# Kernel optimization log

Hardware: AMD Instinct MI355X
Metric: run time of the kernel (lower is better)

Reference implementation:

```python
import jax, jax.numpy as jnp
import numpy as np

B, S, E, H = 4, 2048, 1024, 16
D = E // H  # head_dim = 64


def setup_inputs() -> dict:
    key = jax.random.key(0)
    k1, k2, k3 = jax.random.split(key, 3)
    x = jax.random.normal(k1, (B, S, E), dtype=jnp.float32)
    w_attn = jax.random.normal(k2, (E, 3 * E), dtype=jnp.float32) * (E ** -0.5)
    b_attn = jnp.zeros((3 * E,), dtype=jnp.float32)
    w_out = jax.random.normal(k3, (E, E), dtype=jnp.float32) * (E ** -0.5)
    b_out = jnp.zeros((E,), dtype=jnp.float32)
    return {"x": x, "w_attn": w_attn, "b_attn": b_attn, "w_out": w_out, "b_out": b_out}


def reference(x, w_attn, b_attn, w_out, b_out):
    b, s, e = x.shape
    qkv = x @ w_attn + b_attn                      # [b, s, 3e]
    q, k, v = jnp.split(qkv, 3, axis=2)
    q = q.reshape(b, s, H, D)
    k = k.reshape(b, s, H, D)
    v = v.reshape(b, s, H, D)
    energy = jnp.einsum('nqhd,nkhd->nhqk', q, k)   # [b, H, s, s]
    causal = jnp.tril(jnp.ones((s, s), dtype=bool))
    energy = jnp.where(causal, energy, -jnp.inf)
    scale = jnp.sqrt(jnp.float32(D))
    attn = jax.nn.softmax(energy / scale, axis=-1)  # dropout_rate=0.0 -> identity
    out = jnp.einsum('nhql,nlhd->nqhd', attn, v).reshape(b, s, e)
    return out @ w_out + b_out
```

## Files before the change

### kernel.cpp

```cpp
#include <hip/hip_runtime.h>

typedef short bf16x8 __attribute__((ext_vector_type(8)));
typedef float f32x4 __attribute__((ext_vector_type(4)));
typedef float f32x16 __attribute__((ext_vector_type(16)));
typedef float float4v __attribute__((ext_vector_type(4)));
typedef short short4v __attribute__((ext_vector_type(4)));
typedef unsigned uint2v __attribute__((ext_vector_type(2)));
typedef unsigned uint4v __attribute__((ext_vector_type(4)));

#define B_ 4
#define S_ 2048
#define E_ 1024
#define H_ 16
#define D_ 64
#define M_ (B_*S_)
#define N1_ (3*E_)

__device__ inline short f2bs(float f) {
    unsigned u = __builtin_bit_cast(unsigned, f);
    unsigned r = u + 0x7fffu + ((u >> 16) & 1u);
    return (short)(r >> 16);
}
__device__ inline float exp2a(float x) {
    float r; asm("v_exp_f32 %0, %1" : "=v"(r) : "v"(x)); return r;
}
__device__ inline unsigned cvtpk(float a, float b) {
    unsigned r; asm("v_cvt_pk_bf16_f32 %0, %1, %2" : "=v"(r) : "v"(a), "v"(b)); return r;
}

__device__ inline const __attribute__((address_space(1))) void* gas(const void* p) {
    return (const __attribute__((address_space(1))) void*)p;
}
__device__ inline __attribute__((address_space(3))) void* las(void* p) {
    return (__attribute__((address_space(3))) void*)p;
}

__global__ void convert_f32_bf16(const float* __restrict__ in, short* __restrict__ out, int n) {
    int tid = blockIdx.x * blockDim.x + threadIdx.x;
    int stride = gridDim.x * blockDim.x;
    for (int i = tid * 4; i < n; i += stride * 4) {
        float4v v = *(const float4v*)&in[i];
        short4v o;
        o[0] = f2bs(v[0]); o[1] = f2bs(v[1]); o[2] = f2bs(v[2]); o[3] = f2bs(v[3]);
        *(short4v*)&out[i] = o;
    }
}

__global__ void transpose_convert(const float* __restrict__ in, short* __restrict__ out,
                                  int rows, int cols) {
    __shared__ float t[32][33];
    int bx = blockIdx.x * 32;
    int by = blockIdx.y * 32;
    int tx = threadIdx.x, ty = threadIdx.y;
#pragma unroll
    for (int i = 0; i < 4; ++i)
        t[ty + i * 8][tx] = in[(size_t)(by + ty + i * 8) * cols + bx + tx];
    __syncthreads();
#pragma unroll
    for (int i = 0; i < 4; ++i)
        out[(size_t)(bx + ty + i * 8) * rows + by + tx] = f2bs(t[tx][ty + i * 8]);
}

#define MFMA16(Q) \
    _Pragma("unroll") for (int mf = 0; mf < 2; ++mf) \
    _Pragma("unroll") for (int nf = 0; nf < 4; ++nf) { \
        acc[(Q)*2+mf][nf] = __builtin_amdgcn_mfma_f32_16x16x32_bf16(af[mf][0], bfrag[nf][0], acc[(Q)*2+mf][nf], 0, 0, 0); \
        acc[(Q)*2+mf][nf] = __builtin_amdgcn_mfma_f32_16x16x32_bf16(af[mf][1], bfrag[nf][1], acc[(Q)*2+mf][nf], 0, 0, 0); \
    }

#define PHASE(Q, STAGE_STMT, WAITV) do { \
    bf16x8 af[2][2]; \
    _Pragma("unroll") for (int mf = 0; mf < 2; ++mf) \
    _Pragma("unroll") for (int ks = 0; ks < 2; ++ks) { \
        int r = (Q)*32 + mf*16 + li; \
        af[mf][ks] = *(const bf16x8*)(lA + r*128 + ((ks*64 + g*16) ^ ((r & 7) << 4))); \
    } \
    STAGE_STMT; \
    __builtin_amdgcn_s_barrier(); \
    asm volatile("s_waitcnt lgkmcnt(0)" ::: "memory"); \
    __builtin_amdgcn_sched_barrier(0); \
    __builtin_amdgcn_s_setprio(1); \
    MFMA16(Q); \
    __builtin_amdgcn_s_setprio(0); \
    WAITV; \
    __builtin_amdgcn_s_barrier(); \
} while (0)

#define VMW(n) asm volatile("s_waitcnt vmcnt(" #n ")" ::: "memory")
#define NOP_ ((void)0)

__global__ __launch_bounds__(512, 2) void gemm256_qkv(
    const short* __restrict__ A, const short* __restrict__ Bt,
    const float* __restrict__ bias,
    short* __restrict__ Qb, short* __restrict__ Kb, short* __restrict__ Vt) {
    __shared__ __attribute__((aligned(16))) short lds[2][2][2][8192];
    const int tid = threadIdx.x;
    const int lane = tid & 63;
    const int wid = tid >> 6;
    const int li = lane & 15, g = lane >> 4;
    const int wr = wid >> 2, wc = wid & 3;
    const int Kdim = E_;
    const int NT = Kdim >> 6;

    const int id = blockIdx.x;
    const int swz = (id & 7) * 48 + (id >> 3);
    const int bx = swz % 12, by = swz / 12;
    const int row0 = by * 256, col0 = bx * 256;

    const int rstage = wid * 8 + (lane >> 3);
    const int cstage = (((lane & 7) ^ ((lane >> 3) & 7)) << 4);

    auto stageA = [&](int buf, int kt, int seg) {
#pragma unroll
        for (int h = 0; h < 2; ++h) {
            const char* src = (const char*)A +
                ((size_t)(row0 + h * 128 + seg * 64 + rstage) * Kdim + kt * 64) * 2 + cstage;
            char* dst = (char*)&lds[buf][0][h][0] + seg * 8192 + wid * 1024;
            __builtin_amdgcn_global_load_lds(gas(src), las(dst), 16, 0, 0);
        }
    };
    auto stageB = [&](int buf, int kt, int h) {
#pragma unroll
        for (int seg = 0; seg < 2; ++seg) {
            const char* src = (const char*)Bt +
                ((size_t)(col0 + h * 128 + seg * 64 + rstage) * Kdim + kt * 64) * 2 + cstage;
            char* dst = (char*)&lds[buf][1][h][0] + seg * 8192 + wid * 1024;
            __builtin_amdgcn_global_load_lds(gas(src), las(dst), 16, 0, 0);
        }
    };

    f32x4 acc[8][4];
#pragma unroll
    for (int m = 0; m < 8; ++m)
#pragma unroll
        for (int n = 0; n < 4; ++n) acc[m][n] = (f32x4){0.f, 0.f, 0.f, 0.f};

    stageB(0, 0, 0);
    stageB(0, 0, 1);
    stageA(0, 0, 0);
    stageA(0, 0, 1);
    asm volatile("s_waitcnt vmcnt(0)" ::: "memory");
    __syncthreads();

    const int bc = (wc & 1) * 64;
    for (int t = 0; t < NT; ++t) {
        const int cur = t & 1;
        const int nb = cur ^ 1;
        const int tn = t + 1;
        const bool st = (tn < NT);
        const char* lA = (const char*)&lds[cur][0][wr][0];
        const char* lB = (const char*)&lds[cur][1][wc >> 1][0];

        bf16x8 bfrag[4][2];
#pragma unroll
        for (int nf = 0; nf < 4; ++nf)
#pragma unroll
            for (int ks = 0; ks < 2; ++ks) {
                int r = bc + nf * 16 + li;
                bfrag[nf][ks] = *(const bf16x8*)(lB + r * 128 + ((ks * 64 + g * 16) ^ ((r & 7) << 4)));
            }
        if (st) {
            PHASE(0, stageB(nb, tn, 0), NOP_);
            PHASE(1, stageB(nb, tn, 1), VMW(4));
            PHASE(2, stageA(nb, tn, 0), NOP_);
            PHASE(3, stageA(nb, tn, 1), VMW(2));
        } else {
            PHASE(0, NOP_, NOP_);
            PHASE(1, NOP_, VMW(0));
            PHASE(2, NOP_, NOP_);
            PHASE(3, NOP_, NOP_);
        }
    }

    if (col0 < 2048) {
        short* Dst = (col0 < 1024) ? Qb : Kb;
#pragma unroll
        for (int nf = 0; nf < 4; ++nf) {
            int ncolg = col0 + wc * 64 + nf * 16 + li;
            float bv = bias[ncolg];
            int ncol = ncolg & 1023;
#pragma unroll
            for (int mi = 0; mi < 8; ++mi) {
                int rbase = row0 + wr * 128 + mi * 16 + 4 * g;
#pragma unroll
                for (int j = 0; j < 4; ++j)
                    Dst[(size_t)(rbase + j) * E_ + ncol] = f2bs(acc[mi][nf][j] + bv);
            }
        }
    } else {
#pragma unroll
        for (int nf = 0; nf < 4; ++nf) {
            int ncolg = col0 + wc * 64 + nf * 16 + li;
            float bv = bias[ncolg];
            int rem = ncolg & 1023;
            int h = rem >> 6, d = rem & 63;
#pragma unroll
            for (int mi = 0; mi < 8; ++mi) {
                int s0 = row0 + wr * 128 + mi * 16 + 4 * g;
                int bb2 = s0 >> 11;
                int ss = s0 & 2047;
                uint2v p;
                p[0] = cvtpk(acc[mi][nf][0] + bv, acc[mi][nf][1] + bv);
                p[1] = cvtpk(acc[mi][nf][2] + bv, acc[mi][nf][3] + bv);
                *(uint2v*)&Vt[((size_t)(bb2 * H_ + h) * D_ + d) * S_ + ss] = p;
            }
        }
    }
}

__global__ __launch_bounds__(256, 2) void gemm_bt_out(
    const short* __restrict__ A, const short* __restrict__ Bt,
    const float* __restrict__ bias, float* __restrict__ Cf,
    int Kdim, int Ndim) {
    __shared__ __attribute__((aligned(16))) short As[128 * 32];
    __shared__ __attribute__((aligned(16))) short Bs[128 * 32];
    const int lane = threadIdx.x & 63;
    const int wv = threadIdx.x >> 6;
    const int row0 = blockIdx.y * 128;
    const int col0 = blockIdx.x * 128;
    const int wr = (wv >> 1) * 64;
    const int wc = (wv & 1) * 64;
    const int li = lane & 15;
    const int g = lane >> 4;
    const int lr = lane >> 2;
    const int lk = (lane & 3) * 8;

    f32x4 acc[4][4];
#pragma unroll
    for (int m = 0; m < 4; ++m)
#pragma unroll
        for (int n = 0; n < 4; ++n) acc[m][n] = (f32x4){0.f, 0.f, 0.f, 0.f};

    for (int k0 = 0; k0 < Kdim; k0 += 32) {
#pragma unroll
        for (int i = 0; i < 2; ++i) {
            int cc = wv * 2 + i;
            const short* ga = A + (size_t)(row0 + cc * 16 + lr) * Kdim + k0 + lk;
            __builtin_amdgcn_global_load_lds(gas(ga), las(&As[cc * 512]), 16, 0, 0);
            const short* gb = Bt + (size_t)(col0 + cc * 16 + lr) * Kdim + k0 + lk;
            __builtin_amdgcn_global_load_lds(gas(gb), las(&Bs[cc * 512]), 16, 0, 0);
        }
        __syncthreads();
        bf16x8 af[4], bfr[4];
#pragma unroll
        for (int m = 0; m < 4; ++m) af[m] = *(const bf16x8*)&As[(wr + 16 * m + li) * 32 + g * 8];
#pragma unroll
        for (int n = 0; n < 4; ++n) bfr[n] = *(const bf16x8*)&Bs[(wc + 16 * n + li) * 32 + g * 8];
#pragma unroll
        for (int m = 0; m < 4; ++m)
#pragma unroll
            for (int n = 0; n < 4; ++n)
                acc[m][n] = __builtin_amdgcn_mfma_f32_16x16x32_bf16(af[m], bfr[n], acc[m][n], 0, 0, 0);
        __syncthreads();
    }

#pragma unroll
    for (int n = 0; n < 4; ++n) {
        int ncol = col0 + wc + 16 * n + li;
        float bv = bias[ncol];
#pragma unroll
        for (int m = 0; m < 4; ++m) {
            int rbase = row0 + wr + 16 * m + 4 * g;
#pragma unroll
            for (int j = 0; j < 4; ++j)
                Cf[(size_t)(rbase + j) * Ndim + ncol] = acc[m][n][j] + bv;
        }
    }
}

__global__ __launch_bounds__(256, 4) void attn_kernel(
    const short* __restrict__ Qb, const short* __restrict__ Kb,
    const short* __restrict__ Vt, short* __restrict__ Ob) {
    __shared__ __attribute__((aligned(16))) short Kl[4096];
    __shared__ __attribute__((aligned(16))) short Vl[4096];
    const int lane = threadIdx.x & 63;
    const int wv = threadIdx.x >> 6;
    const int l31 = lane & 31;
    const int hi = lane >> 5;
    const int id = blockIdx.x;
    const int xcd = id & 7;
    const int r_ = id >> 3;
    const int qt = 15 - (r_ >> 3);
    const int bh = xcd * 8 + (r_ & 7);
    const int bb = bh >> 4, hh = bh & 15;
    const short* Qh = Qb + (size_t)bb * (S_ * E_) + hh * 64;
    const short* Kh = Kb + (size_t)bb * (S_ * E_) + hh * 64;
    const short* Vh = Vt + (size_t)bh * (D_ * S_);
    const float CEXP = 0.18033688011112042f;

    const int rstage = wv * 8 + (lane >> 3);
    const int cstage = (((lane & 7) ^ ((lane >> 3) & 7)) << 4);

    const int q0w = qt * 128 + wv * 32;
    const int q = q0w + l31;

    bf16x8 qf[4];
#pragma unroll
    for (int c = 0; c < 4; ++c)
        qf[c] = *(const bf16x8*)&Qh[(size_t)q * E_ + c * 16 + hi * 8];

    f32x16 acc[2];
#pragma unroll
    for (int d = 0; d < 2; ++d)
#pragma unroll
        for (int r = 0; r < 16; ++r) acc[d][r] = 0.f;
    float m = -3e38f, mC = 0.f, l = 0.f;

    const int nw = (q0w + 95) >> 6;
    const int nt = (qt * 128 + 191) >> 6;

    for (int it = 0; it < nt; ++it) {
        const int kt0 = it * 64;
#pragma unroll
        for (int half = 0; half < 2; ++half) {
            const char* gk = (const char*)(Kh + (size_t)(kt0 + half * 32 + rstage) * E_) + cstage;
            __builtin_amdgcn_global_load_lds(gas(gk), las((char*)Kl + half * 4096 + wv * 1024), 16, 0, 0);
            const char* gv = (const char*)Vh + (size_t)(half * 32 + rstage) * (S_ * 2) + (size_t)kt0 * 2 + cstage;
            __builtin_amdgcn_global_load_lds(gas(gv), las((char*)Vl + half * 4096 + wv * 1024), 16, 0, 0);
        }
        __syncthreads();
        if (it < nw) {
#pragma unroll
            for (int s = 0; s < 2; ++s) {
                const int ktl = kt0 + s * 32;
                if (ktl > q0w + 31) continue;
                f32x16 sc;
#pragma unroll
                for (int r = 0; r < 16; ++r) sc[r] = 0.f;
#pragma unroll
                for (int c = 0; c < 4; ++c) {
                    const int row = s * 32 + l31;
                    bf16x8 kf = *(const bf16x8*)((const char*)Kl + row * 128 +
                                                 ((c * 32 + hi * 16) ^ ((row & 7) << 4)));
                    sc = __builtin_amdgcn_mfma_f32_32x32x16_bf16(kf, qf[c], sc, 0, 0, 0);
                }
                if (ktl + 31 > q0w) {
                    const int kb = ktl + 4 * hi;
#pragma unroll
                    for (int r = 0; r < 16; ++r) {
                        int key = kb + (r & 3) + 8 * (r >> 2);
                        sc[r] = (key > q) ? -3e38f : sc[r];
                    }
                }
                float t0 = fmaxf(sc[0], sc[1]), t1 = fmaxf(sc[2], sc[3]);
                float t2 = fmaxf(sc[4], sc[5]), t3 = fmaxf(sc[6], sc[7]);
                float t4 = fmaxf(sc[8], sc[9]), t5 = fmaxf(sc[10], sc[11]);
                float t6 = fmaxf(sc[12], sc[13]), t7 = fmaxf(sc[14], sc[15]);
                float tm = fmaxf(fmaxf(fmaxf(t0, t1), fmaxf(t2, t3)),
                                 fmaxf(fmaxf(t4, t5), fmaxf(t6, t7)));
                tm = fmaxf(tm, __shfl_xor(tm, 32, 64));
                bool need = (tm > m);
                if (__ballot((int)need) != 0ull) {
                    float mn = fmaxf(m, tm);
                    float sf = exp2a((m - mn) * CEXP);
                    m = mn; mC = mn * CEXP;
                    l *= sf;
#pragma unroll
                    for (int d = 0; d < 2; ++d)
#pragma unroll
                        for (int r = 0; r < 16; ++r) acc[d][r] *= sf;
                }
                float p[16];
#pragma unroll
                for (int r = 0; r < 16; ++r) p[r] = exp2a(fmaf(sc[r], CEXP, -mC));
                float s0 = (p[0] + p[1]) + (p[2] + p[3]);
                float s1 = (p[4] + p[5]) + (p[6] + p[7]);
                float s2 = (p[8] + p[9]) + (p[10] + p[11]);
                float s3 = (p[12] + p[13]) + (p[14] + p[15]);
                float ls = (s0 + s1) + (s2 + s3);
                ls += __shfl_xor(ls, 32, 64);
                l += ls;
                unsigned W0 = cvtpk(p[0], p[1]),  W1 = cvtpk(p[2], p[3]);
                unsigned W2 = cvtpk(p[4], p[5]),  W3 = cvtpk(p[6], p[7]);
                unsigned W4 = cvtpk(p[8], p[9]),  W5 = cvtpk(p[10], p[11]);
                unsigned W6 = cvtpk(p[12], p[13]), W7 = cvtpk(p[14], p[15]);
                unsigned xW0 = __shfl_xor(W0, 32, 64), xW1 = __shfl_xor(W1, 32, 64);
                unsigned xW2 = __shfl_xor(W2, 32, 64), xW3 = __shfl_xor(W3, 32, 64);
                unsigned xW4 = __shfl_xor(W4, 32, 64), xW5 = __shfl_xor(W5, 32, 64);
                unsigned xW6 = __shfl_xor(W6, 32, 64), xW7 = __shfl_xor(W7, 32, 64);
                const bool lo = (hi == 0);
                uint4v u1, u2;
                u1[0] = lo ? W0 : xW2;  u1[1] = lo ? W1 : xW3;
                u1[2] = lo ? xW0 : W2;  u1[3] = lo ? xW1 : W3;
                u2[0] = lo ? W4 : xW6;  u2[1] = lo ? W5 : xW7;
                u2[2] = lo ? xW4 : W6;  u2[3] = lo ? xW5 : W7;
                bf16x8 pf1 = __builtin_bit_cast(bf16x8, u1);
                bf16x8 pf2 = __builtin_bit_cast(bf16x8, u2);
#pragma unroll
                for (int db = 0; db < 2; ++db) {
                    const int row = db * 32 + l31;
                    const int rsw = (row & 7) << 4;
                    bf16x8 vf0 = *(const bf16x8*)((const char*)Vl + row * 128 +
                                                  ((s * 64 + hi * 16) ^ rsw));
                    bf16x8 vf1 = *(const bf16x8*)((const char*)Vl + row * 128 +
                                                  ((s * 64 + 32 + hi * 16) ^ rsw));
                    acc[db] = __builtin_amdgcn_mfma_f32_32x32x16_bf16(vf0, pf1, acc[db], 0, 0, 0);
                    acc[db] = __builtin_amdgcn_mfma_f32_32x32x16_bf16(vf1, pf2, acc[db], 0, 0, 0);
                }
            }
        }
        __syncthreads();
    }

    float rl = __builtin_amdgcn_rcpf(l);
    short* orow = Ob + ((size_t)(bb * S_ + q)) * E_ + hh * 64;
#pragma unroll
    for (int db = 0; db < 2; ++db)
#pragma unroll
        for (int rb = 0; rb < 4; ++rb) {
            uint2v pk;
            pk[0] = cvtpk(acc[db][rb * 4 + 0] * rl, acc[db][rb * 4 + 1] * rl);
            pk[1] = cvtpk(acc[db][rb * 4 + 2] * rl, acc[db][rb * 4 + 3] * rl);
            *(uint2v*)&orow[db * 32 + rb * 8 + hi * 4] = pk;
        }
}

extern "C" void kernel_launch(void* const* d_in, const int* in_sizes, int n_in,
                              void* d_out, int out_size, void* d_ws, size_t ws_size,
                              hipStream_t stream) {
    const float* x      = (const float*)d_in[0];
    const float* w_attn = (const float*)d_in[1];
    const float* b_attn = (const float*)d_in[2];
    const float* w_out  = (const float*)d_in[3];
    const float* b_out  = (const float*)d_in[4];
    float* out = (float*)d_out;

    char* ws = (char*)d_ws;
    short* Xbf  = (short*)(ws);
    short* Wat  = (short*)(ws + (16ull << 20));
    short* Wot  = (short*)(ws + (22ull << 20));
    short* Qb   = (short*)(ws + (24ull << 20));
    short* Kb   = (short*)(ws + (40ull << 20));
    short* Vt   = (short*)(ws + (56ull << 20));
    short* Obuf = Xbf;

    convert_f32_bf16<<<2048, 256, 0, stream>>>(x, Xbf, M_ * E_);
    transpose_convert<<<dim3(N1_ / 32, E_ / 32), dim3(32, 8), 0, stream>>>(w_attn, Wat, E_, N1_);
    transpose_convert<<<dim3(E_ / 32, E_ / 32), dim3(32, 8), 0, stream>>>(w_out, Wot, E_, E_);

    gemm256_qkv<<<384, 512, 0, stream>>>(Xbf, Wat, b_attn, Qb, Kb, Vt);

    attn_kernel<<<1024, 256, 0, stream>>>(Qb, Kb, Vt, Obuf);

    gemm_bt_out<<<dim3(E_ / 128, M_ / 128), 256, 0, stream>>>(
        Obuf, Wot, b_out, out, E_, E_);
}
```

Before: 184.3 us.

## Process 64-key tile in one softmax step with lazy max rescaling

The attention inner loop now computes scores for both 32-key halves of the 64-key tile together. It does one max reduction and one online-softmax update per tile instead of one per half, then issues all PV MFMAs back to back. The rescale condition is relaxed to trigger only when the new max exceeds the running max by more than 16, which skips most accumulator rescales. The trade-offs are that fully masked second halves are no longer skipped, register pressure rises, and unrescaled exponents can grow to about 2^(16*CEXP) before a rescale.

```diff
diff --git a/kernel.cpp b/kernel.cpp
--- a/kernel.cpp
+++ b/kernel.cpp
@@ -320,83 +320,95 @@
         }
         __syncthreads();
         if (it < nw) {
+            f32x16 sc0, sc1;
+#pragma unroll
+            for (int r = 0; r < 16; ++r) { sc0[r] = 0.f; sc1[r] = 0.f; }
+#pragma unroll
+            for (int c = 0; c < 4; ++c) {
+                const int r0 = l31, r1 = 32 + l31;
+                bf16x8 kf0 = *(const bf16x8*)((const char*)Kl + r0 * 128 +
+                                              ((c * 32 + hi * 16) ^ ((r0 & 7) << 4)));
+                bf16x8 kf1 = *(const bf16x8*)((const char*)Kl + r1 * 128 +
+                                              ((c * 32 + hi * 16) ^ ((r1 & 7) << 4)));
+                sc0 = __builtin_amdgcn_mfma_f32_32x32x16_bf16(kf0, qf[c], sc0, 0, 0, 0);
+                sc1 = __builtin_amdgcn_mfma_f32_32x32x16_bf16(kf1, qf[c], sc1, 0, 0, 0);
+            }
+            if (kt0 + 63 > q0w) {
+                const int kb = kt0 + 4 * hi;
+#pragma unroll
+                for (int r = 0; r < 16; ++r) {
+                    int key = kb + (r & 3) + 8 * (r >> 2);
+                    sc0[r] = (key > q) ? -3e38f : sc0[r];
+                    sc1[r] = (key + 32 > q) ? -3e38f : sc1[r];
+                }
+            }
+            float tmx[8];
+#pragma unroll
+            for (int r = 0; r < 8; ++r)
+                tmx[r] = fmaxf(fmaxf(sc0[2 * r], sc0[2 * r + 1]),
+                               fmaxf(sc1[2 * r], sc1[2 * r + 1]));
+            float tm = fmaxf(fmaxf(fmaxf(tmx[0], tmx[1]), fmaxf(tmx[2], tmx[3])),
+                             fmaxf(fmaxf(tmx[4], tmx[5]), fmaxf(tmx[6], tmx[7])));
+            tm = fmaxf(tm, __shfl_xor(tm, 32, 64));
+            bool need = (tm > m + 16.0f);
+            if (__ballot((int)need) != 0ull) {
+                float mn = fmaxf(m, tm);
+                float sf = exp2a((m - mn) * CEXP);
+                m = mn; mC = mn * CEXP;
+                l *= sf;
+#pragma unroll
+                for (int d = 0; d < 2; ++d)
+#pragma unroll
+                    for (int r = 0; r < 16; ++r) acc[d][r] *= sf;
+            }
+#pragma unroll
+            for (int r = 0; r < 16; ++r) {
+                sc0[r] = exp2a(fmaf(sc0[r], CEXP, -mC));
+                sc1[r] = exp2a(fmaf(sc1[r], CEXP, -mC));
+            }
+            float s0 = 0.f, s1 = 0.f;
+#pragma unroll
+            for (int r = 0; r < 8; ++r) {
+                s0 += sc0[2 * r] + sc0[2 * r + 1];
+                s1 += sc1[2 * r] + sc1[2 * r + 1];
+            }
+            float ls = s0 + s1;
+            ls += __shfl_xor(ls, 32, 64);
+            l += ls;
+            const bool lo = (hi == 0);
+            bf16x8 pf[4];
 #pragma unroll
             for (int s = 0; s < 2; ++s) {
-                const int ktl = kt0 + s * 32;
-                if (ktl > q0w + 31) continue;
-                f32x16 sc;
-#pragma unroll
-                for (int r = 0; r < 16; ++r) sc[r] = 0.f;
-#pragma unroll
-                for (int c = 0; c < 4; ++c) {
-                    const int row = s * 32 + l31;
-                    bf16x8 kf = *(const bf16x8*)((const char*)Kl + row * 128 +
-                                                 ((c * 32 + hi * 16) ^ ((row & 7) << 4)));
-                    sc = __builtin_amdgcn_mfma_f32_32x32x16_bf16(kf, qf[c], sc, 0, 0, 0);
-                }
-                if (ktl + 31 > q0w) {
-                    const int kb = ktl + 4 * hi;
-#pragma unroll
-                    for (int r = 0; r < 16; ++r) {
-                        int key = kb + (r & 3) + 8 * (r >> 2);
-                        sc[r] = (key > q) ? -3e38f : sc[r];
-                    }
-                }
-                float t0 = fmaxf(sc[0], sc[1]), t1 = fmaxf(sc[2], sc[3]);
-                float t2 = fmaxf(sc[4], sc[5]), t3 = fmaxf(sc[6], sc[7]);
-                float t4 = fmaxf(sc[8], sc[9]), t5 = fmaxf(sc[10], sc[11]);
-                float t6 = fmaxf(sc[12], sc[13]), t7 = fmaxf(sc[14], sc[15]);
-                float tm = fmaxf(fmaxf(fmaxf(t0, t1), fmaxf(t2, t3)),
-                                 fmaxf(fmaxf(t4, t5), fmaxf(t6, t7)));
-                tm = fmaxf(tm, __shfl_xor(tm, 32, 64));
-                bool need = (tm > m);
-                if (__ballot((int)need) != 0ull) {
-                    float mn = fmaxf(m, tm);
-                    float sf = exp2a((m - mn) * CEXP);
-                    m = mn; mC = mn * CEXP;
-                    l *= sf;
-#pragma unroll
-                    for (int d = 0; d < 2; ++d)
-#pragma unroll
-                        for (int r = 0; r < 16; ++r) acc[d][r] *= sf;
-                }
-                float p[16];
-#pragma unroll
-                for (int r = 0; r < 16; ++r) p[r] = exp2a(fmaf(sc[r], CEXP, -mC));
-                float s0 = (p[0] + p[1]) + (p[2] + p[3]);
-                float s1 = (p[4] + p[5]) + (p[6] + p[7]);
-                float s2 = (p[8] + p[9]) + (p[10] + p[11]);
-                float s3 = (p[12] + p[13]) + (p[14] + p[15]);
-                float ls = (s0 + s1) + (s2 + s3);
-                ls += __shfl_xor(ls, 32, 64);
-                l += ls;
-                unsigned W0 = cvtpk(p[0], p[1]),  W1 = cvtpk(p[2], p[3]);
-                unsigned W2 = cvtpk(p[4], p[5]),  W3 = cvtpk(p[6], p[7]);
-                unsigned W4 = cvtpk(p[8], p[9]),  W5 = cvtpk(p[10], p[11]);
+                const f32x16& p = s ? sc1 : sc0;
+                unsigned W0 = cvtpk(p[0], p[1]),   W1 = cvtpk(p[2], p[3]);
+                unsigned W2 = cvtpk(p[4], p[5]),   W3 = cvtpk(p[6], p[7]);
+                unsigned W4 = cvtpk(p[8], p[9]),   W5 = cvtpk(p[10], p[11]);
                 unsigned W6 = cvtpk(p[12], p[13]), W7 = cvtpk(p[14], p[15]);
                 unsigned xW0 = __shfl_xor(W0, 32, 64), xW1 = __shfl_xor(W1, 32, 64);
                 unsigned xW2 = __shfl_xor(W2, 32, 64), xW3 = __shfl_xor(W3, 32, 64);
                 unsigned xW4 = __shfl_xor(W4, 32, 64), xW5 = __shfl_xor(W5, 32, 64);
                 unsigned xW6 = __shfl_xor(W6, 32, 64), xW7 = __shfl_xor(W7, 32, 64);
-                const bool lo = (hi == 0);
                 uint4v u1, u2;
                 u1[0] = lo ? W0 : xW2;  u1[1] = lo ? W1 : xW3;
                 u1[2] = lo ? xW0 : W2;  u1[3] = lo ? xW1 : W3;
                 u2[0] = lo ? W4 : xW6;  u2[1] = lo ? W5 : xW7;
                 u2[2] = lo ? xW4 : W6;  u2[3] = lo ? xW5 : W7;
-                bf16x8 pf1 = __builtin_bit_cast(bf16x8, u1);
-                bf16x8 pf2 = __builtin_bit_cast(bf16x8, u2);
-#pragma unroll
-                for (int db = 0; db < 2; ++db) {
-                    const int row = db * 32 + l31;
-                    const int rsw = (row & 7) << 4;
-                    bf16x8 vf0 = *(const bf16x8*)((const char*)Vl + row * 128 +
-                                                  ((s * 64 + hi * 16) ^ rsw));
-                    bf16x8 vf1 = *(const bf16x8*)((const char*)Vl + row * 128 +
-                                                  ((s * 64 + 32 + hi * 16) ^ rsw));
-                    acc[db] = __builtin_amdgcn_mfma_f32_32x32x16_bf16(vf0, pf1, acc[db], 0, 0, 0);
-                    acc[db] = __builtin_amdgcn_mfma_f32_32x32x16_bf16(vf1, pf2, acc[db], 0, 0, 0);
-                }
+                pf[s * 2] = __builtin_bit_cast(bf16x8, u1);
+                pf[s * 2 + 1] = __builtin_bit_cast(bf16x8, u2);
+            }
+#pragma unroll
+            for (int db = 0; db < 2; ++db) {
+                const int row = db * 32 + l31;
+                const int rsw = (row & 7) << 4;
+                const char* vrow = (const char*)Vl + row * 128;
+                bf16x8 v0 = *(const bf16x8*)(vrow + ((hi * 16) ^ rsw));
+                bf16x8 v1 = *(const bf16x8*)(vrow + ((32 + hi * 16) ^ rsw));
+                bf16x8 v2 = *(const bf16x8*)(vrow + ((64 + hi * 16) ^ rsw));
+                bf16x8 v3 = *(const bf16x8*)(vrow + ((96 + hi * 16) ^ rsw));
+                acc[db] = __builtin_amdgcn_mfma_f32_32x32x16_bf16(v0, pf[0], acc[db], 0, 0, 0);
+                acc[db] = __builtin_amdgcn_mfma_f32_32x32x16_bf16(v1, pf[1], acc[db], 0, 0, 0);
+                acc[db] = __builtin_amdgcn_mfma_f32_32x32x16_bf16(v2, pf[2], acc[db], 0, 0, 0);
+                acc[db] = __builtin_amdgcn_mfma_f32_32x32x16_bf16(v3, pf[3], acc[db], 0, 0, 0);
             }
         }
         __syncthreads();
```

Result: faster. 177.0 us (-4.0%).
